# Kernel tuning notes

Measured on AMD Instinct MI355X. Metric: run time of the kernel, lower is better.

The kernel has to match this reference:

```python
import jax, jax.numpy as jnp
import numpy as np

HEIGHT, WIDTH = 32, 32
NUM_HEADS = 16
FREQUENCY = 10000.0


def _get_thetas(dim, height, width, frequency):
    # dim = head_dim, must be even. Returns (height*width, dim).
    half = dim // 2
    ifreq = 1.0 / (frequency ** (jnp.arange(half, dtype=jnp.float32) / half))
    freqs_h = jnp.arange(height, dtype=jnp.float32)[:, None] * ifreq[None, :]  # (h, half)
    freqs_w = jnp.arange(width, dtype=jnp.float32)[:, None] * ifreq[None, :]   # (w, half)
    theta_h = jnp.broadcast_to(freqs_h[:, None, :], (height, width, half))
    theta_w = jnp.broadcast_to(freqs_w[None, :, :], (height, width, half))
    theta = jnp.concatenate([theta_h, theta_w], axis=-1)  # (h, w, dim)
    return theta.reshape(height * width, dim)


def _add_rope(t, cos, sin):
    # t: (b, h, n, d); cos/sin: (n, d) broadcast over batch and heads
    x1, x2 = jnp.split(t, 2, axis=-1)
    t_rot = jnp.concatenate([-x2, x1], axis=-1)
    return t * cos + t_rot * sin


def setup_inputs() -> dict:
    key = jax.random.key(0)
    k1, k2, k3 = jax.random.split(key, 3)
    b, n, c = 8, HEIGHT * WIDTH, 1024
    tensor = jax.random.normal(k1, (b, n, c), dtype=jnp.float32)
    w_qkv = jax.random.normal(k2, (3 * c, c), dtype=jnp.float32) * (c ** -0.5)
    w_proj = jax.random.normal(k3, (c, c), dtype=jnp.float32) * (c ** -0.5)
    return {"tensor": tensor, "w_qkv": w_qkv, "w_proj": w_proj}


def reference(tensor, w_qkv, w_proj):
    b, n, c = tensor.shape
    hd = c // NUM_HEADS
    # QKV projection, split per-head last dim into q,k,v (matches torch chunk on dim=-1)
    qkv = jnp.einsum('bnc,fc->bnf', tensor, w_qkv)            # (b, n, 3c)
    qkv = qkv.reshape(b, n, NUM_HEADS, 3 * hd).transpose(0, 2, 1, 3)  # (b, H, n, 3*hd)
    q, k, v = jnp.split(qkv, 3, axis=-1)                      # each (b, H, n, hd)
    # 2D RoPE on q, k
    theta = _get_thetas(hd, HEIGHT, WIDTH, FREQUENCY).astype(tensor.dtype)  # (n, hd)
    cos, sin = jnp.cos(theta), jnp.sin(theta)
    q = _add_rope(q, cos, sin)
    k = _add_rope(k, cos, sin)
    # scaled dot product attention
    scale = hd ** -0.5
    scores = jnp.einsum('bhqd,bhkd->bhqk', q, k) * scale
    attn = jax.nn.softmax(scores, axis=-1)
    o = jnp.einsum('bhqk,bhkd->bhqd', attn, v)
    o = o.transpose(0, 2, 1, 3).reshape(b, n, c)
    return jnp.einsum('bnc,oc->bno', o, w_proj)
```

## Files before the change

### kernel.cpp

```cpp
#include <hip/hip_runtime.h>

typedef __attribute__((ext_vector_type(8))) short short8v;
typedef __attribute__((ext_vector_type(4))) float floatx4;
typedef __attribute__((ext_vector_type(4))) unsigned short ushortx4;

__device__ __forceinline__ unsigned int f2bf(float f){
  unsigned int u = __float_as_uint(f);
  u += 0x7fffu + ((u >> 16) & 1u);
  return u >> 16;
}

__device__ __forceinline__ void gload_lds16(const void* g, void* l){
  __builtin_amdgcn_global_load_lds((const __attribute__((address_space(1))) void*)g,
                                   (__attribute__((address_space(3))) void*)l, 16, 0, 0);
}

__global__ __launch_bounds__(256) void prep(
    const floatx4* __restrict__ t,  ushortx4* __restrict__ dt,
    const floatx4* __restrict__ wq, ushortx4* __restrict__ dq,
    const floatx4* __restrict__ wp, ushortx4* __restrict__ dp,
    float2* __restrict__ cs)
{
  int i = blockIdx.x * 256 + threadIdx.x;
  if(i < 3145728){
    const floatx4* s; ushortx4* d; int j;
    if(i < 2097152){ s = t;  d = dt; j = i; }
    else if(i < 2883584){ s = wq; d = dq; j = i - 2097152; }
    else { s = wp; d = dp; j = i - 2883584; }
    floatx4 v = s[j];
    ushortx4 o;
    #pragma unroll
    for(int k = 0; k < 4; ++k) o[k] = (unsigned short)f2bf(v[k]);
    d[j] = o;
  } else {
    int j = i - 3145728;
    int p = j >> 6, dd = j & 63;
    int y = p >> 5, x = p & 31;
    int dm = dd & 31;
    float ifr = powf(10000.0f, -(float)dm * (1.0f / 32.0f));
    float th = (float)(dd < 32 ? y : x) * ifr;
    cs[j].x = cosf(th);
    cs[j].y = sinf(th);
  }
}

template<int EPI>
__global__ __launch_bounds__(512, 2) void gemm8(
    const unsigned short* __restrict__ A,
    const unsigned short* __restrict__ B,
    int K, int N, int NXB,
    float* __restrict__ Cf,
    const float2* __restrict__ cs,
    unsigned short* __restrict__ qw,
    unsigned short* __restrict__ kw,
    unsigned short* __restrict__ vtw)
{
  __shared__ char lds[98304];
  const int tid = threadIdx.x;
  const int w = tid >> 6, lane = tid & 63;
  const int g = lane >> 4, c0 = lane & 15;
  const int wm = w >> 2, wn = w & 3;
  const int NT = K >> 6;

  const int per = gridDim.x >> 3;
  const int wg = (blockIdx.x & 7) * per + (blockIdx.x >> 3);
  const int by = wg / NXB, bx = wg % NXB;
  const size_t m0 = (size_t)by * 128;
  const size_t n0 = (size_t)bx * 256;

  const int row0 = tid >> 2;
  const int xch = (tid & 3) ^ ((tid >> 3) & 3);
  const unsigned short* sA0 = A + (m0 + row0) * K + xch * 8;
  const unsigned short* sB0 = B + (n0 + row0) * K + xch * 8;
  const unsigned short* sB1 = B + (n0 + row0 + 128) * K + xch * 8;
  char* const Ald = lds;
  char* const Bld = lds + 32768;
  const int wb = w * 1024;

  auto stA = [&](int t, int buf, int kh){
    gload_lds16(sA0 + t * 64 + kh * 32, Ald + buf * 16384 + kh * 8192 + wb);
  };
  auto stB = [&](int t, int buf, int kh){
    char* d = Bld + buf * 32768 + kh * 16384 + wb;
    gload_lds16(sB0 + t * 64 + kh * 32, d);
    gload_lds16(sB1 + t * 64 + kh * 32, d + 8192);
  };

  const int archy = (g ^ ((c0 >> 1) & 3)) << 4;
  auto rdA = [&](int buf, int kh, int mf) -> short8v {
    return *(const short8v*)(Ald + buf * 16384 + kh * 8192 +
                             (wm * 64 + mf * 16 + c0) * 64 + archy);
  };
  auto rdB = [&](int buf, int kh, int nf) -> short8v {
    return *(const short8v*)(Bld + buf * 32768 + kh * 16384 +
                             (wn * 64 + nf * 16 + c0) * 64 + archy);
  };

  floatx4 acc[4][4] = {};

#define BARX() do{ __builtin_amdgcn_s_barrier(); __builtin_amdgcn_sched_barrier(0); }while(0)

  auto tile2 = [&](int t, int buf){
    const int ob = buf ^ 1;
    const int tn1 = (t + 1 < NT) ? t + 1 : NT - 1;
    const int tn2 = (t + 2 < NT) ? t + 2 : NT - 1;
    short8v amA[4], bnA[4], amB[4], bnB[4];
    #pragma unroll
    for(int nf = 0; nf < 4; ++nf) bnA[nf] = rdB(buf, 0, nf);
    #pragma unroll
    for(int mf = 0; mf < 4; ++mf) amA[mf] = rdA(buf, 0, mf);
    #pragma unroll
    for(int nf = 0; nf < 4; ++nf) bnB[nf] = rdB(buf, 1, nf);
    #pragma unroll
    for(int mf = 0; mf < 4; ++mf) amB[mf] = rdA(buf, 1, mf);
    stA(tn1, ob, 1); stB(tn1, ob, 1);
    __builtin_amdgcn_sched_barrier(0);
    BARX();
    __builtin_amdgcn_s_setprio(1);
    #pragma unroll
    for(int mf = 0; mf < 4; ++mf)
      #pragma unroll
      for(int nf = 0; nf < 4; ++nf)
        acc[mf][nf] = __builtin_amdgcn_mfma_f32_16x16x32_bf16(amA[mf], bnA[nf], acc[mf][nf], 0, 0, 0);
    __builtin_amdgcn_s_setprio(0);
    stA(tn2, buf, 0); stB(tn2, buf, 0);
    __builtin_amdgcn_s_setprio(1);
    #pragma unroll
    for(int mf = 0; mf < 4; ++mf)
      #pragma unroll
      for(int nf = 0; nf < 4; ++nf)
        acc[mf][nf] = __builtin_amdgcn_mfma_f32_16x16x32_bf16(amB[mf], bnB[nf], acc[mf][nf], 0, 0, 0);
    __builtin_amdgcn_s_setprio(0);
    asm volatile("s_waitcnt vmcnt(3)" ::: "memory");
    BARX();
  };

  stA(0, 0, 0); stB(0, 0, 0);
  stA(0, 0, 1); stB(0, 0, 1);
  stA(1, 1, 0); stB(1, 1, 0);
  asm volatile("s_waitcnt vmcnt(3)" ::: "memory");
  BARX();

  for(int t = 0; t < NT; t += 2){ tile2(t, 0); tile2(t + 1, 1); }
  __syncthreads();
#undef BARX

  if(EPI == 0){
    #pragma unroll
    for(int mf = 0; mf < 4; ++mf){
      size_t mrow = m0 + wm * 64 + mf * 16 + g * 4;
      #pragma unroll
      for(int nf = 0; nf < 4; ++nf){
        size_t n = n0 + wn * 64 + nf * 16 + c0;
        #pragma unroll
        for(int r = 0; r < 4; ++r)
          Cf[(mrow + r) * N + n] = acc[mf][nf][r];
      }
    }
  } else {
    int t = (int)(n0 >> 6) + wn;
    int sect = t % 3, hh = t / 3;
    if(sect == 2){
      #pragma unroll
      for(int mf = 0; mf < 4; ++mf){
        size_t m = m0 + wm * 64 + mf * 16 + g * 4;
        int b = (int)(m >> 10); int p = (int)(m & 1023);
        #pragma unroll
        for(int nf = 0; nf < 4; ++nf){
          int d = nf * 16 + c0;
          ushortx4 pk;
          #pragma unroll
          for(int r = 0; r < 4; ++r) pk[r] = (unsigned short)f2bf(acc[mf][nf][r]);
          *(ushortx4*)(vtw + ((size_t)(b * 16 + hh) * 64 + d) * 1024 + p) = pk;
        }
      }
    } else {
      unsigned short* dst = (sect == 0) ? qw : kw;
      const float qs = (sect == 0) ? 0.18033688011112042f : 1.0f;
      const int codd = c0 & 1;
      #pragma unroll
      for(int mf = 0; mf < 4; ++mf){
        #pragma unroll
        for(int r = 0; r < 4; ++r){
          size_t m = m0 + wm * 64 + mf * 16 + g * 4 + r;
          int b = (int)(m >> 10); int p = (int)(m & 1023);
          const float2* csr = cs + (size_t)p * 64;
          unsigned short* orow = dst + ((size_t)(b * 16 + hh) * 1024 + p) * 64;
          #pragma unroll
          for(int nf = 0; nf < 2; ++nf){
            int d = nf * 16 + c0;
            float x1 = acc[mf][nf][r], x2 = acc[mf][nf + 2][r];
            float2 cc1 = csr[d], cc2 = csr[d + 32];
            unsigned int u1 = f2bf((x1 * cc1.x - x2 * cc1.y) * qs);
            unsigned int u2 = f2bf((x2 * cc2.x + x1 * cc2.y) * qs);
            unsigned int p1 = (unsigned int)__shfl_xor((int)u1, 1);
            unsigned int p2 = (unsigned int)__shfl_xor((int)u2, 1);
            unsigned int val = codd ? (p2 | (u2 << 16)) : (u1 | (p1 << 16));
            int off = codd ? (d + 31) : d;
            *(unsigned int*)(orow + off) = val;
          }
        }
      }
    }
  }
}

__global__ __launch_bounds__(512, 4) void attn_kernel(
    const unsigned short* __restrict__ qw,
    const unsigned short* __restrict__ kw,
    const unsigned short* __restrict__ vtw,
    unsigned short* __restrict__ ow)
{
  __shared__ char smem[65536];
  const int tid = threadIdx.x;
  const int w = tid >> 6, lane = tid & 63;
  const int g = lane >> 4, c0 = lane & 15;
  const int bb = blockIdx.x;
  const int xcd = bb & 7, slot = bb >> 3;
  const int bh = xcd + ((slot >> 2) << 3);
  const int qt = slot & 3;
  const size_t bhoff = (size_t)bh * 1024 * 64;
  const unsigned short* Qb = qw + bhoff;
  const unsigned short* Kb = kw + bhoff;
  const unsigned short* Vb = vtw + bhoff;
  const int q0 = qt * 256 + w * 32;
  char* Pw = smem + 32768 + w * 4096;

  const int srow = tid >> 3;
  const int sjx = ((tid & 7) ^ (srow & 7)) << 3;
  const unsigned short* ksrc = Kb + srow * 64 + sjx;
  const unsigned short* vsrc = Vb + (size_t)srow * 1024 + sjx;
  const int wbase = w * 1024;

  short8v bq[2][2];
  #pragma unroll
  for(int qf = 0; qf < 2; ++qf)
    #pragma unroll
    for(int i = 0; i < 2; ++i)
      bq[qf][i] = *(const short8v*)(Qb + (size_t)(q0 + qf * 16 + c0) * 64 + g * 8 + i * 32);

  floatx4 o[2][4] = {};
  float m_run[2] = {-1e30f, -1e30f};
  float l_part[2] = {0.0f, 0.0f};

  gload_lds16(ksrc, smem + wbase);
  gload_lds16(vsrc, smem + 8192 + wbase);
  __syncthreads();

  int cur = 0;
  for(int kv0 = 0; kv0 < 1024; kv0 += 64){
    char* Ksm = smem + cur * 16384;
    char* Vsm = smem + cur * 16384 + 8192;
    if(kv0 + 64 < 1024){
      char* alt = smem + (cur ^ 1) * 16384;
      gload_lds16(ksrc + (size_t)(kv0 + 64) * 64, alt + wbase);
      gload_lds16(vsrc + kv0 + 64, alt + 8192 + wbase);
    }
    floatx4 st[4][2];
    #pragma unroll
    for(int kf = 0; kf < 4; ++kf){
      const int krow = kf * 16 + c0;
      const char* kr = Ksm + (krow << 7);
      short8v ka0 = *(const short8v*)(kr + (((g    ) ^ (c0 & 7)) << 4));
      short8v ka1 = *(const short8v*)(kr + (((g + 4) ^ (c0 & 7)) << 4));
      #pragma unroll
      for(int qf = 0; qf < 2; ++qf){
        floatx4 z = {};
        z = __builtin_amdgcn_mfma_f32_16x16x32_bf16(ka0, bq[qf][0], z, 0, 0, 0);
        st[kf][qf] = __builtin_amdgcn_mfma_f32_16x16x32_bf16(ka1, bq[qf][1], z, 0, 0, 0);
      }
    }
    float vmax[2];
    #pragma unroll
    for(int qf = 0; qf < 2; ++qf){
      float vm = -1e30f;
      #pragma unroll
      for(int kf = 0; kf < 4; ++kf)
        #pragma unroll
        for(int r = 0; r < 4; ++r) vm = fmaxf(vm, st[kf][qf][r]);
      vm = fmaxf(vm, __shfl_xor(vm, 16));
      vm = fmaxf(vm, __shfl_xor(vm, 32));
      vmax[qf] = vm;
    }
    if(!__all(vmax[0] <= m_run[0] + 8.0f && vmax[1] <= m_run[1] + 8.0f)){
      #pragma unroll
      for(int qf = 0; qf < 2; ++qf){
        float m_new = fmaxf(m_run[qf], vmax[qf]);
        float sc = __builtin_amdgcn_exp2f(m_run[qf] - m_new);
        l_part[qf] *= sc;
        m_run[qf] = m_new;
        float f0 = __shfl(sc, g * 4 + 0);
        float f1 = __shfl(sc, g * 4 + 1);
        float f2 = __shfl(sc, g * 4 + 2);
        float f3 = __shfl(sc, g * 4 + 3);
        #pragma unroll
        for(int nf = 0; nf < 4; ++nf){
          o[qf][nf][0] *= f0; o[qf][nf][1] *= f1; o[qf][nf][2] *= f2; o[qf][nf][3] *= f3;
        }
      }
    }
    #pragma unroll
    for(int qf = 0; qf < 2; ++qf){
      float ps = 0.0f;
      #pragma unroll
      for(int kf = 0; kf < 4; ++kf){
        ushortx4 pk;
        #pragma unroll
        for(int r = 0; r < 4; ++r){
          float e = __builtin_amdgcn_exp2f(st[kf][qf][r] - m_run[qf]);
          ps += e;
          pk[r] = (unsigned short)f2bf(e);
        }
        int byo = (qf << 11) + (c0 << 7) + (kf << 5) + (g << 3);
        byo ^= (c0 & 7) << 4;
        *(ushortx4*)(Pw + byo) = pk;
      }
      l_part[qf] += ps;
    }
    short8v pa[2][2];
    #pragma unroll
    for(int mf = 0; mf < 2; ++mf)
      #pragma unroll
      for(int i = 0; i < 2; ++i){
        int byo = (mf << 11) + (c0 << 7) + (i << 6) + (g << 4);
        byo ^= (c0 & 7) << 4;
        pa[mf][i] = *(const short8v*)(Pw + byo);
      }
    #pragma unroll
    for(int nf = 0; nf < 4; ++nf){
      const int vrow = nf * 16 + c0;
      const char* vr = Vsm + (vrow << 7);
      short8v v0 = *(const short8v*)(vr + (((g    ) ^ (c0 & 7)) << 4));
      short8v v1 = *(const short8v*)(vr + (((g + 4) ^ (c0 & 7)) << 4));
      #pragma unroll
      for(int mf = 0; mf < 2; ++mf){
        o[mf][nf] = __builtin_amdgcn_mfma_f32_16x16x32_bf16(pa[mf][0], v0, o[mf][nf], 0, 0, 0);
        o[mf][nf] = __builtin_amdgcn_mfma_f32_16x16x32_bf16(pa[mf][1], v1, o[mf][nf], 0, 0, 0);
      }
    }
    __syncthreads();
    cur ^= 1;
  }

  const int b = bh >> 4, hh = bh & 15;
  #pragma unroll
  for(int mf = 0; mf < 2; ++mf){
    l_part[mf] += __shfl_xor(l_part[mf], 16);
    l_part[mf] += __shfl_xor(l_part[mf], 32);
    float i0 = 1.0f / __shfl(l_part[mf], g * 4 + 0);
    float i1 = 1.0f / __shfl(l_part[mf], g * 4 + 1);
    float i2 = 1.0f / __shfl(l_part[mf], g * 4 + 2);
    float i3 = 1.0f / __shfl(l_part[mf], g * 4 + 3);
    #pragma unroll
    for(int nf = 0; nf < 4; ++nf){
      o[mf][nf][0] *= i0; o[mf][nf][1] *= i1; o[mf][nf][2] *= i2; o[mf][nf][3] *= i3;
      #pragma unroll
      for(int r = 0; r < 4; ++r){
        size_t row = (size_t)b * 1024 + q0 + mf * 16 + g * 4 + r;
        ow[row * 1024 + hh * 64 + nf * 16 + c0] = (unsigned short)f2bf(o[mf][nf][r]);
      }
    }
  }
}


extern "C" void kernel_launch(void* const* d_in, const int* in_sizes, int n_in,
                              void* d_out, int out_size, void* d_ws, size_t ws_size,
                              hipStream_t stream){
  const float* tensor = (const float*)d_in[0];
  const float* w_qkv  = (const float*)d_in[1];
  const float* w_proj = (const float*)d_in[2];
  char* ws = (char*)d_ws;
  unsigned short* bfT  = (unsigned short*)(ws);
  unsigned short* bfWq = (unsigned short*)(ws + 16777216);
  unsigned short* bfWp = (unsigned short*)(ws + 23068672);
  float2*         cs   = (float2*)        (ws + 25165824);
  unsigned short* qw   = (unsigned short*)(ws + 25690112);
  unsigned short* kw   = (unsigned short*)(ws + 42467328);
  unsigned short* vtw  = (unsigned short*)(ws + 59244544);
  unsigned short* owp  = (unsigned short*)(ws + 76021760);

  prep<<<12544, 256, 0, stream>>>((const floatx4*)tensor, (ushortx4*)bfT,
                                  (const floatx4*)w_qkv,  (ushortx4*)bfWq,
                                  (const floatx4*)w_proj, (ushortx4*)bfWp, cs);

  gemm8<1><<<768, 512, 0, stream>>>(bfT, bfWq, 1024, 3072, 12,
                                    nullptr, cs, qw, kw, vtw);
  attn_kernel<<<512, 512, 0, stream>>>(qw, kw, vtw, owp);
  gemm8<0><<<256, 512, 0, stream>>>(owp, bfWp, 1024, 1024, 4,
                                    (float*)d_out, nullptr, nullptr, nullptr, nullptr);
}
```

Baseline: 161.2 us.

## Triple-buffer GEMM LDS tiles with a single barrier per K-step

The GEMM main loop moves from a double-buffered LDS scheme, which staged each K-tile in two halves and needed two barriers per tile, to a three-slot rotating buffer. Each tile is now loaded whole, two tiles ahead, and there is one vmcnt wait plus one barrier per iteration. The aim is to cut barrier stalls and give global-to-LDS loads more time in flight behind the MFMA work. In exchange, LDS use grows from 96KB to 144KB per block, which could limit blocks per CU, and the priority window around the MFMAs changes.

```diff
diff --git a/kernel.cpp b/kernel.cpp
--- a/kernel.cpp
+++ b/kernel.cpp
@@ -55,7 +55,7 @@
     unsigned short* __restrict__ kw,
     unsigned short* __restrict__ vtw)
 {
-  __shared__ char lds[98304];
+  __shared__ char lds[147456];
   const int tid = threadIdx.x;
   const int w = tid >> 6, lane = tid & 63;
   const int g = lane >> 4, c0 = lane & 15;
@@ -73,77 +73,67 @@
   const unsigned short* sA0 = A + (m0 + row0) * K + xch * 8;
   const unsigned short* sB0 = B + (n0 + row0) * K + xch * 8;
   const unsigned short* sB1 = B + (n0 + row0 + 128) * K + xch * 8;
-  char* const Ald = lds;
-  char* const Bld = lds + 32768;
   const int wb = w * 1024;
 
-  auto stA = [&](int t, int buf, int kh){
-    gload_lds16(sA0 + t * 64 + kh * 32, Ald + buf * 16384 + kh * 8192 + wb);
+  auto stT = [&](int t, char* bp){
+    gload_lds16(sA0 + t * 64,      bp + wb);
+    gload_lds16(sA0 + t * 64 + 32, bp + 8192 + wb);
+    gload_lds16(sB0 + t * 64,      bp + 16384 + wb);
+    gload_lds16(sB1 + t * 64,      bp + 24576 + wb);
+    gload_lds16(sB0 + t * 64 + 32, bp + 32768 + wb);
+    gload_lds16(sB1 + t * 64 + 32, bp + 40960 + wb);
   };
-  auto stB = [&](int t, int buf, int kh){
-    char* d = Bld + buf * 32768 + kh * 16384 + wb;
-    gload_lds16(sB0 + t * 64 + kh * 32, d);
-    gload_lds16(sB1 + t * 64 + kh * 32, d + 8192);
+
+  const int archy = (g ^ ((c0 >> 1) & 3)) << 4;
+  auto rdA = [&](const char* bp, int kh, int mf) -> short8v {
+    return *(const short8v*)(bp + kh * 8192 + (wm * 64 + mf * 16 + c0) * 64 + archy);
   };
-
-  const int archy = (g ^ ((c0 >> 1) & 3)) << 4;
-  auto rdA = [&](int buf, int kh, int mf) -> short8v {
-    return *(const short8v*)(Ald + buf * 16384 + kh * 8192 +
-                             (wm * 64 + mf * 16 + c0) * 64 + archy);
+  auto rdB = [&](const char* bp, int kh, int nf) -> short8v {
+    return *(const short8v*)(bp + 16384 + kh * 16384 + (wn * 64 + nf * 16 + c0) * 64 + archy);
   };
-  auto rdB = [&](int buf, int kh, int nf) -> short8v {
-    return *(const short8v*)(Bld + buf * 32768 + kh * 16384 +
-                             (wn * 64 + nf * 16 + c0) * 64 + archy);
-  };
 
   floatx4 acc[4][4] = {};
 
-#define BARX() do{ __builtin_amdgcn_s_barrier(); __builtin_amdgcn_sched_barrier(0); }while(0)
-
-  auto tile2 = [&](int t, int buf){
-    const int ob = buf ^ 1;
-    const int tn1 = (t + 1 < NT) ? t + 1 : NT - 1;
+  stT(0, lds);
+  stT(1, lds + 49152);
+  asm volatile("s_waitcnt vmcnt(6)" ::: "memory");
+  __builtin_amdgcn_s_barrier();
+  __builtin_amdgcn_sched_barrier(0);
+
+  char* pa_ = lds;
+  char* pb_ = lds + 49152;
+  char* pc_ = lds + 98304;
+  for(int t = 0; t < NT; ++t){
     const int tn2 = (t + 2 < NT) ? t + 2 : NT - 1;
     short8v amA[4], bnA[4], amB[4], bnB[4];
     #pragma unroll
-    for(int nf = 0; nf < 4; ++nf) bnA[nf] = rdB(buf, 0, nf);
-    #pragma unroll
-    for(int mf = 0; mf < 4; ++mf) amA[mf] = rdA(buf, 0, mf);
-    #pragma unroll
-    for(int nf = 0; nf < 4; ++nf) bnB[nf] = rdB(buf, 1, nf);
-    #pragma unroll
-    for(int mf = 0; mf < 4; ++mf) amB[mf] = rdA(buf, 1, mf);
-    stA(tn1, ob, 1); stB(tn1, ob, 1);
+    for(int nf = 0; nf < 4; ++nf) bnA[nf] = rdB(pa_, 0, nf);
+    #pragma unroll
+    for(int mf = 0; mf < 4; ++mf) amA[mf] = rdA(pa_, 0, mf);
+    #pragma unroll
+    for(int nf = 0; nf < 4; ++nf) bnB[nf] = rdB(pa_, 1, nf);
+    #pragma unroll
+    for(int mf = 0; mf < 4; ++mf) amB[mf] = rdA(pa_, 1, mf);
+    stT(tn2, pc_);
     __builtin_amdgcn_sched_barrier(0);
-    BARX();
     __builtin_amdgcn_s_setprio(1);
     #pragma unroll
     for(int mf = 0; mf < 4; ++mf)
       #pragma unroll
       for(int nf = 0; nf < 4; ++nf)
         acc[mf][nf] = __builtin_amdgcn_mfma_f32_16x16x32_bf16(amA[mf], bnA[nf], acc[mf][nf], 0, 0, 0);
-    __builtin_amdgcn_s_setprio(0);
-    stA(tn2, buf, 0); stB(tn2, buf, 0);
-    __builtin_amdgcn_s_setprio(1);
     #pragma unroll
     for(int mf = 0; mf < 4; ++mf)
       #pragma unroll
       for(int nf = 0; nf < 4; ++nf)
         acc[mf][nf] = __builtin_amdgcn_mfma_f32_16x16x32_bf16(amB[mf], bnB[nf], acc[mf][nf], 0, 0, 0);
     __builtin_amdgcn_s_setprio(0);
-    asm volatile("s_waitcnt vmcnt(3)" ::: "memory");
-    BARX();
-  };
-
-  stA(0, 0, 0); stB(0, 0, 0);
-  stA(0, 0, 1); stB(0, 0, 1);
-  stA(1, 1, 0); stB(1, 1, 0);
-  asm volatile("s_waitcnt vmcnt(3)" ::: "memory");
-  BARX();
-
-  for(int t = 0; t < NT; t += 2){ tile2(t, 0); tile2(t + 1, 1); }
+    asm volatile("s_waitcnt vmcnt(6)" ::: "memory");
+    __builtin_amdgcn_s_barrier();
+    __builtin_amdgcn_sched_barrier(0);
+    char* tmp = pa_; pa_ = pb_; pb_ = pc_; pc_ = tmp;
+  }
   __syncthreads();
-#undef BARX
 
   if(EPI == 0){
     #pragma unroll
```

New measurement: 160.9 us, median of 2. No clear change (-0.2%).

## Split GEMM k-tile into four LDS-read/MFMA phases with interleaved barriers

Applied to the files above, without the earlier changes.

Restructures the GEMM inner loop so each k-tile is processed in four smaller phases. Each phase reads a subset of A/B fragments from LDS, waits on lgkmcnt, then runs 8 MFMAs, and global-to-LDS stores are spread between phases. The intent is to cut register pressure (fragment registers drop from 16 to 6) and to interleave LDS reads with MFMA work across waves, ping-pong style. The cost is several extra workgroup barriers per tile, which could add synchronisation overhead.

```diff
diff --git a/kernel.cpp b/kernel.cpp
--- a/kernel.cpp
+++ b/kernel.cpp
@@ -99,37 +99,59 @@
   floatx4 acc[4][4] = {};
 
 #define BARX() do{ __builtin_amdgcn_s_barrier(); __builtin_amdgcn_sched_barrier(0); }while(0)
-
-  auto tile2 = [&](int t, int buf){
+#define LGKM0() do{ asm volatile("s_waitcnt lgkmcnt(0)" ::: "memory"); \
+                    __builtin_amdgcn_sched_barrier(0); }while(0)
+
+  auto tile4 = [&](int t, int buf){
     const int ob = buf ^ 1;
     const int tn1 = (t + 1 < NT) ? t + 1 : NT - 1;
     const int tn2 = (t + 2 < NT) ? t + 2 : NT - 1;
-    short8v amA[4], bnA[4], amB[4], bnB[4];
-    #pragma unroll
-    for(int nf = 0; nf < 4; ++nf) bnA[nf] = rdB(buf, 0, nf);
-    #pragma unroll
-    for(int mf = 0; mf < 4; ++mf) amA[mf] = rdA(buf, 0, mf);
-    #pragma unroll
-    for(int nf = 0; nf < 4; ++nf) bnB[nf] = rdB(buf, 1, nf);
-    #pragma unroll
-    for(int mf = 0; mf < 4; ++mf) amB[mf] = rdA(buf, 1, mf);
+    short8v am[4], bn[2];
+    #pragma unroll
+    for(int mf = 0; mf < 4; ++mf) am[mf] = rdA(buf, 0, mf);
+    bn[0] = rdB(buf, 0, 0); bn[1] = rdB(buf, 0, 1);
     stA(tn1, ob, 1); stB(tn1, ob, 1);
-    __builtin_amdgcn_sched_barrier(0);
+    BARX(); LGKM0();
+    __builtin_amdgcn_s_setprio(1);
+    #pragma unroll
+    for(int mf = 0; mf < 4; ++mf){
+      acc[mf][0] = __builtin_amdgcn_mfma_f32_16x16x32_bf16(am[mf], bn[0], acc[mf][0], 0, 0, 0);
+      acc[mf][1] = __builtin_amdgcn_mfma_f32_16x16x32_bf16(am[mf], bn[1], acc[mf][1], 0, 0, 0);
+    }
+    __builtin_amdgcn_s_setprio(0);
     BARX();
+    bn[0] = rdB(buf, 0, 2); bn[1] = rdB(buf, 0, 3);
+    BARX(); LGKM0();
     __builtin_amdgcn_s_setprio(1);
     #pragma unroll
-    for(int mf = 0; mf < 4; ++mf)
-      #pragma unroll
-      for(int nf = 0; nf < 4; ++nf)
-        acc[mf][nf] = __builtin_amdgcn_mfma_f32_16x16x32_bf16(amA[mf], bnA[nf], acc[mf][nf], 0, 0, 0);
+    for(int mf = 0; mf < 4; ++mf){
+      acc[mf][2] = __builtin_amdgcn_mfma_f32_16x16x32_bf16(am[mf], bn[0], acc[mf][2], 0, 0, 0);
+      acc[mf][3] = __builtin_amdgcn_mfma_f32_16x16x32_bf16(am[mf], bn[1], acc[mf][3], 0, 0, 0);
+    }
     __builtin_amdgcn_s_setprio(0);
-    stA(tn2, buf, 0); stB(tn2, buf, 0);
+    BARX();
+    #pragma unroll
+    for(int mf = 0; mf < 4; ++mf) am[mf] = rdA(buf, 1, mf);
+    bn[0] = rdB(buf, 1, 0); bn[1] = rdB(buf, 1, 1);
+    stA(tn2, buf, 0);
+    BARX(); LGKM0();
     __builtin_amdgcn_s_setprio(1);
     #pragma unroll
-    for(int mf = 0; mf < 4; ++mf)
-      #pragma unroll
-      for(int nf = 0; nf < 4; ++nf)
-        acc[mf][nf] = __builtin_amdgcn_mfma_f32_16x16x32_bf16(amB[mf], bnB[nf], acc[mf][nf], 0, 0, 0);
+    for(int mf = 0; mf < 4; ++mf){
+      acc[mf][0] = __builtin_amdgcn_mfma_f32_16x16x32_bf16(am[mf], bn[0], acc[mf][0], 0, 0, 0);
+      acc[mf][1] = __builtin_amdgcn_mfma_f32_16x16x32_bf16(am[mf], bn[1], acc[mf][1], 0, 0, 0);
+    }
+    __builtin_amdgcn_s_setprio(0);
+    BARX();
+    bn[0] = rdB(buf, 1, 2); bn[1] = rdB(buf, 1, 3);
+    stB(tn2, buf, 0);
+    BARX(); LGKM0();
+    __builtin_amdgcn_s_setprio(1);
+    #pragma unroll
+    for(int mf = 0; mf < 4; ++mf){
+      acc[mf][2] = __builtin_amdgcn_mfma_f32_16x16x32_bf16(am[mf], bn[0], acc[mf][2], 0, 0, 0);
+      acc[mf][3] = __builtin_amdgcn_mfma_f32_16x16x32_bf16(am[mf], bn[1], acc[mf][3], 0, 0, 0);
+    }
     __builtin_amdgcn_s_setprio(0);
     asm volatile("s_waitcnt vmcnt(3)" ::: "memory");
     BARX();
@@ -141,9 +163,10 @@
   asm volatile("s_waitcnt vmcnt(3)" ::: "memory");
   BARX();
 
-  for(int t = 0; t < NT; t += 2){ tile2(t, 0); tile2(t + 1, 1); }
+  for(int t = 0; t < NT; t += 2){ tile4(t, 0); tile4(t + 1, 1); }
   __syncthreads();
 #undef BARX
+#undef LGKM0
 
   if(EPI == 0){
     #pragma unroll
```

Result: no change. 163.9 us (+1.7%).
